# Performance work log

Measured on AMD Instinct MI355X. Metric: run time of the kernel, lower is better.

Reference implementation:

```python
import jax, jax.numpy as jnp
import numpy as np

N_NODES = 50000
N_EDGES = 800000
D_IN = 64
D_OUT = 64


def setup_inputs() -> dict:
    key = jax.random.key(0)
    k1, k2, k3 = jax.random.split(key, 3)
    x = jax.random.normal(k1, (N_NODES, D_IN), dtype=jnp.float32)
    edge_index = jax.random.randint(k2, (2, N_EDGES), 0, N_NODES, dtype=jnp.int64)
    # xavier_uniform for weight [in, out]
    limit = np.sqrt(6.0 / (D_IN + D_OUT)).astype(np.float32)
    weight = jax.random.uniform(k3, (D_IN, D_OUT), dtype=jnp.float32, minval=-limit, maxval=limit)
    bias = jnp.zeros((D_OUT,), dtype=jnp.float32)
    return {"x": x, "edge_index": edge_index, "weight": weight, "bias": bias}


def reference(x, edge_index, weight, bias):
    n = x.shape[0]
    # add self loops
    loops = jnp.arange(n, dtype=edge_index.dtype)
    row = jnp.concatenate([edge_index[0], loops])  # [E+N]
    col = jnp.concatenate([edge_index[1], loops])  # [E+N]
    # degree over row (as in torch_geometric degree(row, N))
    deg = jax.ops.segment_sum(jnp.ones_like(row, dtype=x.dtype), row, num_segments=n)
    deg_inv_sqrt = jnp.where(deg > 0, jax.lax.rsqrt(deg), jnp.zeros_like(deg))
    norm = deg_inv_sqrt[row] * deg_inv_sqrt[col]  # [E+N]
    h = x @ weight  # [N, D_OUT]
    # gather-scale-scatter: out[col] += h[row] * norm
    out = jax.ops.segment_sum(h[row] * norm[:, None], col, num_segments=n)
    return out + bias
```

## Files before the change

### kernel.cpp

```cpp
#include <hip/hip_runtime.h>
#include <hip/hip_bf16.h>


constexpr int N_NODES = 50000;
constexpr int N_EDGES = 800000;
constexpr int D = 64;
constexpr int NB_SCAN = (N_NODES + 255) / 256;

constexpr int B_SLICE = 64;
constexpr int SLICE = N_EDGES / B_SLICE;
constexpr int PACK8 = N_NODES / 4;
constexpr int QUAR = N_NODES / 4;

static __device__ __forceinline__ unsigned short f2bf(float f) {
    unsigned u = __float_as_uint(f);
    unsigned r = (u + 0x7fffu + ((u >> 16) & 1u)) >> 16;
    return (unsigned short)r;
}
static __device__ __forceinline__ float bf2f(unsigned short s) {
    return __uint_as_float((unsigned)s << 16);
}

__global__ __launch_bounds__(1024) void hist_priv_kernel(const int* __restrict__ ei,
                                                         unsigned* __restrict__ bh) {
    __shared__ unsigned loc[PACK8];
    int b = blockIdx.x;
    int s = b & (B_SLICE - 1);
    const int* arr = (b < B_SLICE) ? ei : ei + N_EDGES;
    for (int w = threadIdx.x; w < PACK8; w += 1024) loc[w] = 0;
    __syncthreads();
    const int* p = arr + s * SLICE;
    for (int i = threadIdx.x; i < SLICE; i += 1024) {
        int k = p[i];
        atomicAdd(&loc[k >> 2], 1u << (8 * (k & 3)));
    }
    __syncthreads();
    unsigned* dst = bh + (size_t)b * PACK8;
    for (int w = threadIdx.x; w < PACK8; w += 1024) dst[w] = loc[w];
}

__global__ __launch_bounds__(1024) void reduce_scan_kernel(const unsigned* __restrict__ bh,
                                                           float* __restrict__ dis,
                                                           int* __restrict__ offs_local,
                                                           int* __restrict__ partials,
                                                           unsigned char* __restrict__ bs8) {
    __shared__ int degp[4][256];
    __shared__ int colp[4][256];
    __shared__ int s[256];
    const int t = threadIdx.x;
    const int nl = t & 255;
    const int g = t >> 8;
    const int i = blockIdx.x * 256 + nl;

    unsigned lp[16];
    int ct = 0;
    if (i < N_NODES) {
        const int w = i >> 2;
        const unsigned sh = 8 * (i & 3);
        const unsigned* prow = bh + (size_t)(g * 16) * PACK8 + w;
        unsigned vr[16];
#pragma unroll
        for (int k = 0; k < 16; ++k) vr[k] = prow[(size_t)k * PACK8];
        int dl = 0;
#pragma unroll
        for (int k = 0; k < 16; ++k) dl += (int)((vr[k] >> sh) & 0xffu);
        degp[g][nl] = dl;

        const unsigned* pcol = bh + (size_t)(B_SLICE + g * 16) * PACK8 + w;
        unsigned vc[16];
#pragma unroll
        for (int k = 0; k < 16; ++k) vc[k] = pcol[(size_t)k * PACK8];
        unsigned c = 0;
#pragma unroll
        for (int k = 0; k < 16; ++k) { lp[k] = c; c += (vc[k] >> sh) & 0xffu; }
        ct = (int)c;
        colp[g][nl] = ct;
    } else {
        degp[g][nl] = 0;
        colp[g][nl] = 0;
    }
    __syncthreads();

    if (i < N_NODES) {
        int base = 0;
#pragma unroll
        for (int gg = 0; gg < 4; ++gg) if (gg < g) base += colp[gg][nl];
#pragma unroll
        for (int k = 0; k < 16; ++k)
            bs8[(size_t)(g * 16 + k) * N_NODES + i] = (unsigned char)(base + (int)lp[k]);
        if (g == 0) {
            int deg = degp[0][nl] + degp[1][nl] + degp[2][nl] + degp[3][nl];
            dis[i] = rsqrtf((float)deg + 1.0f);
        }
    }
    if (g == 0) s[nl] = colp[0][nl] + colp[1][nl] + colp[2][nl] + colp[3][nl];
    __syncthreads();

    for (int d = 1; d < 256; d <<= 1) {
        int u = (t < 256 && t >= d) ? s[t - d] : 0;
        __syncthreads();
        if (t < 256) s[t] += u;
        __syncthreads();
    }
    if (g == 0 && i < N_NODES) {
        int tot = colp[0][nl] + colp[1][nl] + colp[2][nl] + colp[3][nl];
        offs_local[i] = s[nl] - tot;
    }
    if (t == 255) partials[blockIdx.x] = s[255];
}

__global__ __launch_bounds__(256, 4) void gemm_kernel(const float* __restrict__ x,
                                                      const float* __restrict__ W,
                                                      const float* __restrict__ dis,
                                                      unsigned short* __restrict__ hs,
                                                      const int* __restrict__ offs_local,
                                                      const int* __restrict__ partials,
                                                      int* __restrict__ offs,
                                                      int do_offs) {
    __shared__ float Xs[64][68];
    __shared__ float Ws[64][64];
    __shared__ int pref[256];
    int t = threadIdx.x;
    int b = blockIdx.x;

    if (do_offs && b < NB_SCAN) {
        pref[t] = (t < NB_SCAN) ? partials[t] : 0;
        __syncthreads();
        for (int d = 1; d < 256; d <<= 1) {
            int u = (t >= d) ? pref[t - d] : 0;
            __syncthreads();
            pref[t] += u;
            __syncthreads();
        }
        int base = pref[b] - partials[b];
        int node = b * 256 + t;
        if (node < N_NODES) offs[node] = base + offs_local[node];
        if (b == 0 && t == 0) offs[N_NODES] = N_EDGES;
    }

    int n0 = blockIdx.x * 64;

    const float4* W4 = (const float4*)W;
    float4* Ws4 = (float4*)Ws;
#pragma unroll
    for (int i = 0; i < 4; ++i) Ws4[t + i * 256] = W4[t + i * 256];

    const float4* x4 = (const float4*)(x + (size_t)n0 * D);
#pragma unroll
    for (int i = 0; i < 4; ++i) {
        int f = t + i * 256;
        int r = f >> 4, c = (f & 15) << 2;
        float4 v = make_float4(0.f, 0.f, 0.f, 0.f);
        if (n0 + r < N_NODES) v = x4[f];
        Xs[r][c] = v.x; Xs[r][c + 1] = v.y; Xs[r][c + 2] = v.z; Xs[r][c + 3] = v.w;
    }
    __syncthreads();

    int tx = t & 15, ty = t >> 4;
    float acc[4][4] = {};
#pragma unroll 8
    for (int k = 0; k < D; ++k) {
        float a[4], bb[4];
#pragma unroll
        for (int i = 0; i < 4; ++i) a[i] = Xs[ty * 4 + i][k];
#pragma unroll
        for (int jj = 0; jj < 4; ++jj) bb[jj] = Ws[k][tx * 4 + jj];
#pragma unroll
        for (int i = 0; i < 4; ++i)
#pragma unroll
            for (int jj = 0; jj < 4; ++jj)
                acc[i][jj] = fmaf(a[i], bb[jj], acc[i][jj]);
    }

#pragma unroll
    for (int i = 0; i < 4; ++i) {
        int r = ty * 4 + i;
        if (n0 + r < N_NODES) {
            float dr = dis[n0 + r];
            ushort4 v;
            v.x = f2bf(acc[i][0] * dr); v.y = f2bf(acc[i][1] * dr);
            v.z = f2bf(acc[i][2] * dr); v.w = f2bf(acc[i][3] * dr);
            *(ushort4*)(hs + (size_t)(n0 + r) * D + tx * 4) = v;
        }
    }
}

__global__ __launch_bounds__(1024) void bucket_det_kernel(const int* __restrict__ ei,
                                                          const unsigned char* __restrict__ bs8,
                                                          const int* __restrict__ offs,
                                                          int* __restrict__ csr) {
    __shared__ unsigned pos[QUAR / 4];
    const int t = threadIdx.x;
    const int s = blockIdx.x >> 2;
    const int q = blockIdx.x & 3;
    const int c0 = q * QUAR;

    const unsigned* rel32 = (const unsigned*)(bs8 + (size_t)s * N_NODES + c0);
    for (int w = t; w < QUAR / 4; w += 1024) pos[w] = rel32[w];
    __syncthreads();

    const int* rowp = ei + s * SLICE;
    const int* colp = ei + N_EDGES + s * SLICE;
    for (int i = t; i < SLICE; i += 1024) {
        int c = colp[i];
        unsigned cc = (unsigned)(c - c0);
        if (cc < (unsigned)QUAR) {
            int base = offs[c];
            unsigned old = atomicAdd(&pos[cc >> 2], 1u << (8 * (cc & 3)));
            unsigned rel = (old >> (8 * (cc & 3))) & 0xffu;
            csr[base + (int)rel] = rowp[i];
        }
    }
}

__global__ __launch_bounds__(256) void gather_kernel(const int* __restrict__ offs,
                                                     const int* __restrict__ csr,
                                                     const unsigned short* __restrict__ hs,
                                                     const float* __restrict__ dis,
                                                     const float* __restrict__ bias,
                                                     float* __restrict__ out) {
    int wave = threadIdx.x >> 6;
    int j = threadIdx.x & 63;
    int n = blockIdx.x * 4 + wave;
    if (n >= N_NODES) return;

    float a[8];
    a[0] = bf2f(hs[(size_t)n * D + j]);
#pragma unroll
    for (int k = 1; k < 8; ++k) a[k] = 0.f;

    int beg = __builtin_amdgcn_readfirstlane(offs[n]);
    int m   = __builtin_amdgcn_readfirstlane(offs[n + 1]) - beg;
    const int* p = csr + beg;

    int i = 0;
    for (; i + 16 <= m; i += 16) {
        int r[16];
        float v[16];
#pragma unroll
        for (int k = 0; k < 16; ++k) r[k] = p[i + k];
#pragma unroll
        for (int k = 0; k < 16; ++k) v[k] = bf2f(hs[(size_t)r[k] * D + j]);
#pragma unroll
        for (int k = 0; k < 16; ++k) a[k & 7] += v[k];
    }
    for (; i + 4 <= m; i += 4) {
        int r0 = p[i], r1 = p[i + 1], r2 = p[i + 2], r3 = p[i + 3];
        a[0] += bf2f(hs[(size_t)r0 * D + j]);
        a[1] += bf2f(hs[(size_t)r1 * D + j]);
        a[2] += bf2f(hs[(size_t)r2 * D + j]);
        a[3] += bf2f(hs[(size_t)r3 * D + j]);
    }
    for (; i < m; ++i) a[1] += bf2f(hs[(size_t)p[i] * D + j]);
    float tot = ((a[0] + a[1]) + (a[2] + a[3])) + ((a[4] + a[5]) + (a[6] + a[7]));
    out[(size_t)n * D + j] = fmaf(dis[n], tot, bias[j]);
}


__global__ void histf_kernel(const int* __restrict__ row, const int* __restrict__ col,
                             int* __restrict__ degi, int* __restrict__ cnt) {
    int e = blockIdx.x * blockDim.x + threadIdx.x;
    if (e < N_EDGES) {
        atomicAdd(&degi[row[e]], 1);
        atomicAdd(&cnt[col[e]], 1);
    }
}

__global__ void disf_kernel(int* __restrict__ degi) {
    int i = blockIdx.x * blockDim.x + threadIdx.x;
    if (i < N_NODES) {
        float d = (float)degi[i] + 1.0f;
        ((float*)degi)[i] = rsqrtf(d);
    }
}

__global__ void block_scan_kernel(const int* __restrict__ cnt, int* __restrict__ offs,
                                  int* __restrict__ partials) {
    __shared__ int s[256];
    int t = threadIdx.x;
    int i = blockIdx.x * 256 + t;
    int v = (i < N_NODES) ? cnt[i] : 0;
    s[t] = v;
    __syncthreads();
    for (int d = 1; d < 256; d <<= 1) {
        int u = (t >= d) ? s[t - d] : 0;
        __syncthreads();
        s[t] += u;
        __syncthreads();
    }
    if (i < N_NODES) offs[i] = s[t] - v;
    if (t == 255) partials[blockIdx.x] = s[t];
}

__global__ void scan_partials_kernel(int* __restrict__ partials) {
    __shared__ int s[256];
    int t = threadIdx.x;
    int v = (t < NB_SCAN) ? partials[t] : 0;
    s[t] = v;
    __syncthreads();
    for (int d = 1; d < 256; d <<= 1) {
        int u = (t >= d) ? s[t - d] : 0;
        __syncthreads();
        s[t] += u;
        __syncthreads();
    }
    if (t < NB_SCAN) partials[t] = s[t] - v;
}

__global__ void add_off_kernel(int* __restrict__ offs, const int* __restrict__ partials) {
    int i = blockIdx.x * 256 + threadIdx.x;
    if (i < N_NODES) offs[i] += partials[blockIdx.x];
    if (i == 0) offs[N_NODES] = N_EDGES;
}

__global__ void bucket_fb_kernel(const int* __restrict__ row, const int* __restrict__ col,
                                 const int* __restrict__ offs, int* __restrict__ cur,
                                 int* __restrict__ csr) {
    int e = blockIdx.x * blockDim.x + threadIdx.x;
    if (e < N_EDGES) {
        int c = col[e];
        int pos = offs[c] + atomicAdd(&cur[c], 1);
        csr[pos] = row[e];
    }
}


extern "C" void kernel_launch(void* const* d_in, const int* in_sizes, int n_in,
                              void* d_out, int out_size, void* d_ws, size_t ws_size,
                              hipStream_t stream) {
    const float* x    = (const float*)d_in[0];
    const int*   ei   = (const int*)d_in[1];
    const float* W    = (const float*)d_in[2];
    const float* bias = (const float*)d_in[3];
    float* out = (float*)d_out;

    char* ws = (char*)d_ws;
    float*          dis      = (float*)(ws + 0);
    int*            offs     = (int*)(ws + 200000);
    int*            offs_loc = (int*)(ws + 400064);
    int*            cur      = (int*)(ws + 600064);
    int*            partials = (int*)(ws + 800064);
    int*            csr      = (int*)(ws + 801088);
    unsigned short* hs       = (unsigned short*)(ws + 4001088);
    unsigned*       bh       = (unsigned*)(ws + 10401088);
    unsigned char*  bs8      = (unsigned char*)(ws + 16801088);

    const size_t WS_NEEDED = 20001088;

    if (ws_size >= WS_NEEDED) {
        hist_priv_kernel<<<2 * B_SLICE, 1024, 0, stream>>>(ei, bh);
        reduce_scan_kernel<<<NB_SCAN, 1024, 0, stream>>>(bh, dis, offs_loc, partials, bs8);
        gemm_kernel<<<(N_NODES + 63) / 64, 256, 0, stream>>>(x, W, dis, hs,
                                                             offs_loc, partials, offs, 1);
        bucket_det_kernel<<<4 * B_SLICE, 1024, 0, stream>>>(ei, bs8, offs, csr);
        gather_kernel<<<(N_NODES + 3) / 4, 256, 0, stream>>>(offs, csr, hs, dis, bias, out);
    } else {
        const int* row = ei;
        const int* col = ei + N_EDGES;
        int* degi = (int*)dis;
        int* cntf = offs_loc;
        hipMemsetAsync(ws, 0, 800064, stream);
        histf_kernel<<<(N_EDGES + 255) / 256, 256, 0, stream>>>(row, col, degi, cntf);
        disf_kernel<<<(N_NODES + 255) / 256, 256, 0, stream>>>(degi);
        block_scan_kernel<<<NB_SCAN, 256, 0, stream>>>(cntf, offs, partials);
        scan_partials_kernel<<<1, 256, 0, stream>>>(partials);
        add_off_kernel<<<NB_SCAN, 256, 0, stream>>>(offs, partials);
        gemm_kernel<<<(N_NODES + 63) / 64, 256, 0, stream>>>(x, W, dis, hs,
                                                             offs_loc, partials, offs, 0);
        bucket_fb_kernel<<<(N_EDGES + 255) / 256, 256, 0, stream>>>(row, col, offs, cur, csr);
        gather_kernel<<<(N_NODES + 3) / 4, 256, 0, stream>>>(offs, csr, hs, dis, bias, out);
    }
}
```

Baseline: 127.6 us.

## Fuse GEMM, bucketing and gather into one cooperative kernel with grid sync

Replaces the three launches (gemm, bucket, gather) with a single cooperative kernel of 256 blocks x 1024 threads. Each block first builds the offsets and scatters its CSR bucket, then part of the blocks compute the bf16-scaled X·W tile, a grid-wide sync separates this from the gather/accumulate phase. It aims to remove launch gaps and overlap bucketing with the GEMM, at the cost of a fixed small grid, LDS union pressure, and a grid barrier; the old path stays as a fallback if the cooperative launch fails.

```diff
diff --git a/kernel.cpp b/kernel.cpp
--- a/kernel.cpp
+++ b/kernel.cpp
@@ -1,5 +1,8 @@
 #include <hip/hip_runtime.h>
 #include <hip/hip_bf16.h>
+#include <hip/hip_cooperative_groups.h>
+
+namespace cg = cooperative_groups;
 
 
 constexpr int N_NODES = 50000;
@@ -107,6 +110,172 @@
         offs_local[i] = s[nl] - tot;
     }
     if (t == 255) partials[blockIdx.x] = s[255];
+}
+
+struct TailLds {
+    union {
+        struct {
+            unsigned pos[QUAR / 4];
+            int pref[256];
+        } bk;
+        struct {
+            float Xs[4][64][68];
+            float Ws[64][64];
+        } g;
+    } u;
+};
+
+__global__ __launch_bounds__(1024, 4) void fused_tail_kernel(
+        const int* __restrict__ ei,
+        const int* __restrict__ offs_local,
+        const int* __restrict__ partials,
+        const unsigned char* __restrict__ bs8,
+        const float* __restrict__ x,
+        const float* __restrict__ W,
+        const float* __restrict__ dis,
+        unsigned short* __restrict__ hs,
+        int* __restrict__ csr,
+        int* __restrict__ offs,
+        const float* __restrict__ bias,
+        float* __restrict__ out) {
+    __shared__ TailLds L;
+    const int t = threadIdx.x;
+    const int b = blockIdx.x;
+
+    if (t < 256) L.u.bk.pref[t] = (t < NB_SCAN) ? partials[t] : 0;
+    __syncthreads();
+    for (int d = 1; d < 256; d <<= 1) {
+        int u = 0;
+        if (t < 256 && t >= d) u = L.u.bk.pref[t - d];
+        __syncthreads();
+        if (t < 256) L.u.bk.pref[t] += u;
+        __syncthreads();
+    }
+    if (t < 256) {
+        int inc = L.u.bk.pref[t];
+        int own = (t < NB_SCAN) ? partials[t] : 0;
+        L.u.bk.pref[t] = inc - own;
+    }
+    __syncthreads();
+
+    {
+        const int s = b >> 2;
+        const int q = b & 3;
+        const int c0 = q * QUAR;
+        const unsigned* rel32 = (const unsigned*)(bs8 + (size_t)s * N_NODES + c0);
+        for (int w = t; w < QUAR / 4; w += 1024) L.u.bk.pos[w] = rel32[w];
+        if (s == 0) {
+            const int* olq = offs_local + c0;
+            for (int w = t; w < QUAR; w += 1024) {
+                int node = c0 + w;
+                offs[node] = L.u.bk.pref[node >> 8] + olq[w];
+            }
+            if (q == 3 && t == 0) offs[N_NODES] = N_EDGES;
+        }
+        __syncthreads();
+
+        const int* rowp = ei + s * SLICE;
+        const int* colp = ei + N_EDGES + s * SLICE;
+        for (int i = t; i < SLICE; i += 1024) {
+            int c = colp[i];
+            unsigned cc = (unsigned)(c - c0);
+            if (cc < (unsigned)QUAR) {
+                int base = L.u.bk.pref[c >> 8] + offs_local[c];
+                unsigned old = atomicAdd(&L.u.bk.pos[cc >> 2], 1u << (8 * (cc & 3)));
+                unsigned rel = (old >> (8 * (cc & 3))) & 0xffu;
+                csr[base + (int)rel] = rowp[i];
+            }
+        }
+    }
+    __syncthreads();
+
+    if (b < 196) {
+        const int grp = t >> 8, t256 = t & 255;
+        const int tb = b * 4 + grp;
+        const int n0 = tb * 64;
+
+        ((float4*)L.u.g.Ws)[t] = ((const float4*)W)[t];
+
+        float (*Xs)[68] = L.u.g.Xs[grp];
+        const float4* x4 = (const float4*)(x + (size_t)n0 * D);
+#pragma unroll
+        for (int i = 0; i < 4; ++i) {
+            int f = t256 + i * 256;
+            int r = f >> 4, c = (f & 15) << 2;
+            float4 v = make_float4(0.f, 0.f, 0.f, 0.f);
+            if (n0 + r < N_NODES) v = x4[f];
+            Xs[r][c] = v.x; Xs[r][c + 1] = v.y; Xs[r][c + 2] = v.z; Xs[r][c + 3] = v.w;
+        }
+        __syncthreads();
+
+        int tx = t256 & 15, ty = t256 >> 4;
+        float acc[4][4] = {};
+#pragma unroll 8
+        for (int k = 0; k < D; ++k) {
+            float a[4], bb[4];
+#pragma unroll
+            for (int i = 0; i < 4; ++i) a[i] = Xs[ty * 4 + i][k];
+#pragma unroll
+            for (int jj = 0; jj < 4; ++jj) bb[jj] = L.u.g.Ws[k][tx * 4 + jj];
+#pragma unroll
+            for (int i = 0; i < 4; ++i)
+#pragma unroll
+                for (int jj = 0; jj < 4; ++jj)
+                    acc[i][jj] = fmaf(a[i], bb[jj], acc[i][jj]);
+        }
+
+#pragma unroll
+        for (int i = 0; i < 4; ++i) {
+            int r = ty * 4 + i;
+            if (n0 + r < N_NODES) {
+                float dr = dis[n0 + r];
+                ushort4 v;
+                v.x = f2bf(acc[i][0] * dr); v.y = f2bf(acc[i][1] * dr);
+                v.z = f2bf(acc[i][2] * dr); v.w = f2bf(acc[i][3] * dr);
+                *(ushort4*)(hs + (size_t)(n0 + r) * D + tx * 4) = v;
+            }
+        }
+    }
+
+    __threadfence();
+    cg::this_grid().sync();
+
+    {
+        const int wave = t >> 6;
+        const int j = t & 63;
+        for (int n = b * 16 + wave; n < N_NODES; n += 4096) {
+            float a[8];
+            a[0] = bf2f(hs[(size_t)n * D + j]);
+#pragma unroll
+            for (int k = 1; k < 8; ++k) a[k] = 0.f;
+
+            int beg = __builtin_amdgcn_readfirstlane(offs[n]);
+            int m   = __builtin_amdgcn_readfirstlane(offs[n + 1]) - beg;
+            const int* p = csr + beg;
+
+            int i = 0;
+            for (; i + 16 <= m; i += 16) {
+                int r[16];
+                float v[16];
+#pragma unroll
+                for (int k = 0; k < 16; ++k) r[k] = p[i + k];
+#pragma unroll
+                for (int k = 0; k < 16; ++k) v[k] = bf2f(hs[(size_t)r[k] * D + j]);
+#pragma unroll
+                for (int k = 0; k < 16; ++k) a[k & 7] += v[k];
+            }
+            for (; i + 4 <= m; i += 4) {
+                int r0 = p[i], r1 = p[i + 1], r2 = p[i + 2], r3 = p[i + 3];
+                a[0] += bf2f(hs[(size_t)r0 * D + j]);
+                a[1] += bf2f(hs[(size_t)r1 * D + j]);
+                a[2] += bf2f(hs[(size_t)r2 * D + j]);
+                a[3] += bf2f(hs[(size_t)r3 * D + j]);
+            }
+            for (; i < m; ++i) a[1] += bf2f(hs[(size_t)p[i] * D + j]);
+            float tot = ((a[0] + a[1]) + (a[2] + a[3])) + ((a[4] + a[5]) + (a[6] + a[7]));
+            out[(size_t)n * D + j] = fmaf(dis[n], tot, bias[j]);
+        }
+    }
 }
 
 __global__ __launch_bounds__(256, 4) void gemm_kernel(const float* __restrict__ x,
@@ -350,10 +519,30 @@
     if (ws_size >= WS_NEEDED) {
         hist_priv_kernel<<<2 * B_SLICE, 1024, 0, stream>>>(ei, bh);
         reduce_scan_kernel<<<NB_SCAN, 1024, 0, stream>>>(bh, dis, offs_loc, partials, bs8);
-        gemm_kernel<<<(N_NODES + 63) / 64, 256, 0, stream>>>(x, W, dis, hs,
-                                                             offs_loc, partials, offs, 1);
-        bucket_det_kernel<<<4 * B_SLICE, 1024, 0, stream>>>(ei, bs8, offs, csr);
-        gather_kernel<<<(N_NODES + 3) / 4, 256, 0, stream>>>(offs, csr, hs, dis, bias, out);
+
+        const int*           a_ei   = ei;
+        const int*           a_ol   = offs_loc;
+        const int*           a_pt   = partials;
+        const unsigned char* a_bs8  = bs8;
+        const float*         a_x    = x;
+        const float*         a_W    = W;
+        const float*         a_dis  = dis;
+        unsigned short*      a_hs   = hs;
+        int*                 a_csr  = csr;
+        int*                 a_offs = offs;
+        const float*         a_bias = bias;
+        float*               a_out  = out;
+        void* args[] = {&a_ei, &a_ol, &a_pt, &a_bs8, &a_x, &a_W, &a_dis,
+                        &a_hs, &a_csr, &a_offs, &a_bias, &a_out};
+        hipError_t ce = hipLaunchCooperativeKernel((const void*)fused_tail_kernel,
+                                                   dim3(256), dim3(1024), args, 0, stream);
+        if (ce != hipSuccess) {
+            gemm_kernel<<<(N_NODES + 63) / 64, 256, 0, stream>>>(x, W, dis, hs,
+                                                                 offs_loc, partials, offs, 1);
+            bucket_det_kernel<<<4 * B_SLICE, 1024, 0, stream>>>(ei, bs8, offs, csr);
+            gather_kernel<<<(N_NODES + 3) / 4, 256, 0, stream>>>(offs, csr, hs, dis,
+                                                                 bias, out);
+        }
     } else {
         const int* row = ei;
         const int* col = ei + N_EDGES;
```

Measured after the change: 303.5 us. 2.38x slower.

## Fuse GEMM and CSR bucket fill into one heterogeneous-block kernel

Applied to the files above, without the earlier changes.

Merges the GEMM and the deterministic bucket-fill kernels into a single launch. Blocks are split by index: 512 bucket blocks work on eighth-ranges of destination nodes and the remaining blocks run the GEMM. Each bucket block recomputes the partials prefix scan itself and derives CSR offsets from offs_local plus the block prefix, so it no longer waits on offs written by the GEMM kernel. This removes one launch and lets the GEMM overlap with the atomic-heavy scatter, at the cost of a redundant scan in every bucket block and more ei re-reads from the finer node partitioning.

```diff
diff --git a/kernel.cpp b/kernel.cpp
--- a/kernel.cpp
+++ b/kernel.cpp
@@ -10,7 +10,10 @@
 constexpr int B_SLICE = 64;
 constexpr int SLICE = N_EDGES / B_SLICE;
 constexpr int PACK8 = N_NODES / 4;
-constexpr int QUAR = N_NODES / 4;
+
+constexpr int OCT = 6272;
+constexpr int NB_BUCKET = B_SLICE * 8;
+constexpr int NB_GEMM = (N_NODES + 63) / 64;
 
 static __device__ __forceinline__ unsigned short f2bf(float f) {
     unsigned u = __float_as_uint(f);
@@ -53,7 +56,6 @@
     const int i = blockIdx.x * 256 + nl;
 
     unsigned lp[16];
-    int ct = 0;
     if (i < N_NODES) {
         const int w = i >> 2;
         const unsigned sh = 8 * (i & 3);
@@ -73,8 +75,7 @@
         unsigned c = 0;
 #pragma unroll
         for (int k = 0; k < 16; ++k) { lp[k] = c; c += (vc[k] >> sh) & 0xffu; }
-        ct = (int)c;
-        colp[g][nl] = ct;
+        colp[g][nl] = (int)c;
     } else {
         degp[g][nl] = 0;
         colp[g][nl] = 0;
@@ -109,106 +110,126 @@
     if (t == 255) partials[blockIdx.x] = s[255];
 }
 
-__global__ __launch_bounds__(256, 4) void gemm_kernel(const float* __restrict__ x,
-                                                      const float* __restrict__ W,
-                                                      const float* __restrict__ dis,
-                                                      unsigned short* __restrict__ hs,
-                                                      const int* __restrict__ offs_local,
-                                                      const int* __restrict__ partials,
-                                                      int* __restrict__ offs,
-                                                      int do_offs) {
-    __shared__ float Xs[64][68];
-    __shared__ float Ws[64][64];
-    __shared__ int pref[256];
-    int t = threadIdx.x;
-    int b = blockIdx.x;
-
-    if (do_offs && b < NB_SCAN) {
-        pref[t] = (t < NB_SCAN) ? partials[t] : 0;
+struct FgbLds {
+    union {
+        struct {
+            unsigned pos[OCT / 4];
+            int pref[256];
+        } bk;
+        struct {
+            float Xs[64][68];
+            float Ws[64][64];
+        } g;
+    } u;
+};
+
+__global__ __launch_bounds__(256, 4) void fused_gb_kernel(
+        const float* __restrict__ x,
+        const float* __restrict__ W,
+        const float* __restrict__ dis,
+        unsigned short* __restrict__ hs,
+        const int* __restrict__ ei,
+        const int* __restrict__ offs_local,
+        const int* __restrict__ partials,
+        const unsigned char* __restrict__ bs8,
+        int* __restrict__ csr,
+        int* __restrict__ offs) {
+    __shared__ FgbLds L;
+    const int t = threadIdx.x;
+    const int b = blockIdx.x;
+
+    if (b < NB_BUCKET) {
+        L.u.bk.pref[t] = (t < NB_SCAN) ? partials[t] : 0;
         __syncthreads();
         for (int d = 1; d < 256; d <<= 1) {
-            int u = (t >= d) ? pref[t - d] : 0;
+            int u = (t >= d) ? L.u.bk.pref[t - d] : 0;
             __syncthreads();
-            pref[t] += u;
+            L.u.bk.pref[t] += u;
             __syncthreads();
         }
-        int base = pref[b] - partials[b];
-        int node = b * 256 + t;
-        if (node < N_NODES) offs[node] = base + offs_local[node];
-        if (b == 0 && t == 0) offs[N_NODES] = N_EDGES;
-    }
-
-    int n0 = blockIdx.x * 64;
-
-    const float4* W4 = (const float4*)W;
-    float4* Ws4 = (float4*)Ws;
-#pragma unroll
-    for (int i = 0; i < 4; ++i) Ws4[t + i * 256] = W4[t + i * 256];
-
-    const float4* x4 = (const float4*)(x + (size_t)n0 * D);
-#pragma unroll
-    for (int i = 0; i < 4; ++i) {
-        int f = t + i * 256;
-        int r = f >> 4, c = (f & 15) << 2;
-        float4 v = make_float4(0.f, 0.f, 0.f, 0.f);
-        if (n0 + r < N_NODES) v = x4[f];
-        Xs[r][c] = v.x; Xs[r][c + 1] = v.y; Xs[r][c + 2] = v.z; Xs[r][c + 3] = v.w;
-    }
-    __syncthreads();
-
-    int tx = t & 15, ty = t >> 4;
-    float acc[4][4] = {};
+        {
+            int inc = L.u.bk.pref[t];
+            int own = (t < NB_SCAN) ? partials[t] : 0;
+            L.u.bk.pref[t] = inc - own;
+        }
+        __syncthreads();
+
+        const int s = b >> 3;
+        const int o = b & 7;
+        const int c0 = o * OCT;
+        const int range = (c0 + OCT <= N_NODES) ? OCT : (N_NODES - c0);
+
+        const unsigned* rel32 = (const unsigned*)(bs8 + (size_t)s * N_NODES + c0);
+        for (int w = t; w < range / 4; w += 256) L.u.bk.pos[w] = rel32[w];
+
+        if (s == 0) {
+            const int* olq = offs_local + c0;
+            for (int w = t; w < range; w += 256) {
+                int node = c0 + w;
+                offs[node] = L.u.bk.pref[node >> 8] + olq[w];
+            }
+            if (o == 7 && t == 0) offs[N_NODES] = N_EDGES;
+        }
+        __syncthreads();
+
+        const int* rowp = ei + s * SLICE;
+        const int* colp = ei + N_EDGES + s * SLICE;
+        for (int i = t; i < SLICE; i += 256) {
+            int c = colp[i];
+            unsigned cc = (unsigned)(c - c0);
+            if (cc < (unsigned)range) {
+                int base = L.u.bk.pref[c >> 8] + offs_local[c];
+                unsigned old = atomicAdd(&L.u.bk.pos[cc >> 2], 1u << (8 * (cc & 3)));
+                unsigned rel = (old >> (8 * (cc & 3))) & 0xffu;
+                csr[base + (int)rel] = rowp[i];
+            }
+        }
+    } else {
+        const int n0 = (b - NB_BUCKET) * 64;
+
+        const float4* W4 = (const float4*)W;
+        float4* Ws4 = (float4*)L.u.g.Ws;
+#pragma unroll
+        for (int i = 0; i < 4; ++i) Ws4[t + i * 256] = W4[t + i * 256];
+
+        const float4* x4 = (const float4*)(x + (size_t)n0 * D);
+#pragma unroll
+        for (int i = 0; i < 4; ++i) {
+            int f = t + i * 256;
+            int r = f >> 4, c = (f & 15) << 2;
+            float4 v = make_float4(0.f, 0.f, 0.f, 0.f);
+            if (n0 + r < N_NODES) v = x4[f];
+            L.u.g.Xs[r][c] = v.x; L.u.g.Xs[r][c + 1] = v.y;
+            L.u.g.Xs[r][c + 2] = v.z; L.u.g.Xs[r][c + 3] = v.w;
+        }
+        __syncthreads();
+
+        int tx = t & 15, ty = t >> 4;
+        float acc[4][4] = {};
 #pragma unroll 8
-    for (int k = 0; k < D; ++k) {
-        float a[4], bb[4];
-#pragma unroll
-        for (int i = 0; i < 4; ++i) a[i] = Xs[ty * 4 + i][k];
-#pragma unroll
-        for (int jj = 0; jj < 4; ++jj) bb[jj] = Ws[k][tx * 4 + jj];
-#pragma unroll
-        for (int i = 0; i < 4; ++i)
-#pragma unroll
-            for (int jj = 0; jj < 4; ++jj)
-                acc[i][jj] = fmaf(a[i], bb[jj], acc[i][jj]);
-    }
-
-#pragma unroll
-    for (int i = 0; i < 4; ++i) {
-        int r = ty * 4 + i;
-        if (n0 + r < N_NODES) {
-            float dr = dis[n0 + r];
-            ushort4 v;
-            v.x = f2bf(acc[i][0] * dr); v.y = f2bf(acc[i][1] * dr);
-            v.z = f2bf(acc[i][2] * dr); v.w = f2bf(acc[i][3] * dr);
-            *(ushort4*)(hs + (size_t)(n0 + r) * D + tx * 4) = v;
-        }
-    }
-}
-
-__global__ __launch_bounds__(1024) void bucket_det_kernel(const int* __restrict__ ei,
-                                                          const unsigned char* __restrict__ bs8,
-                                                          const int* __restrict__ offs,
-                                                          int* __restrict__ csr) {
-    __shared__ unsigned pos[QUAR / 4];
-    const int t = threadIdx.x;
-    const int s = blockIdx.x >> 2;
-    const int q = blockIdx.x & 3;
-    const int c0 = q * QUAR;
-
-    const unsigned* rel32 = (const unsigned*)(bs8 + (size_t)s * N_NODES + c0);
-    for (int w = t; w < QUAR / 4; w += 1024) pos[w] = rel32[w];
-    __syncthreads();
-
-    const int* rowp = ei + s * SLICE;
-    const int* colp = ei + N_EDGES + s * SLICE;
-    for (int i = t; i < SLICE; i += 1024) {
-        int c = colp[i];
-        unsigned cc = (unsigned)(c - c0);
-        if (cc < (unsigned)QUAR) {
-            int base = offs[c];
-            unsigned old = atomicAdd(&pos[cc >> 2], 1u << (8 * (cc & 3)));
-            unsigned rel = (old >> (8 * (cc & 3))) & 0xffu;
-            csr[base + (int)rel] = rowp[i];
+        for (int k = 0; k < D; ++k) {
+            float a[4], bb[4];
+#pragma unroll
+            for (int i = 0; i < 4; ++i) a[i] = L.u.g.Xs[ty * 4 + i][k];
+#pragma unroll
+            for (int jj = 0; jj < 4; ++jj) bb[jj] = L.u.g.Ws[k][tx * 4 + jj];
+#pragma unroll
+            for (int i = 0; i < 4; ++i)
+#pragma unroll
+                for (int jj = 0; jj < 4; ++jj)
+                    acc[i][jj] = fmaf(a[i], bb[jj], acc[i][jj]);
+        }
+
+#pragma unroll
+        for (int i = 0; i < 4; ++i) {
+            int r = ty * 4 + i;
+            if (n0 + r < N_NODES) {
+                float dr = dis[n0 + r];
+                ushort4 v;
+                v.x = f2bf(acc[i][0] * dr); v.y = f2bf(acc[i][1] * dr);
+                v.z = f2bf(acc[i][2] * dr); v.w = f2bf(acc[i][3] * dr);
+                *(ushort4*)(hs + (size_t)(n0 + r) * D + tx * 4) = v;
+            }
         }
     }
 }
@@ -256,6 +277,60 @@
     out[(size_t)n * D + j] = fmaf(dis[n], tot, bias[j]);
 }
 
+__global__ __launch_bounds__(256, 4) void gemm_kernel(const float* __restrict__ x,
+                                                      const float* __restrict__ W,
+                                                      const float* __restrict__ dis,
+                                                      unsigned short* __restrict__ hs) {
+    __shared__ float Xs[64][68];
+    __shared__ float Ws[64][64];
+    int t = threadIdx.x;
+    int n0 = blockIdx.x * 64;
+
+    const float4* W4 = (const float4*)W;
+    float4* Ws4 = (float4*)Ws;
+#pragma unroll
+    for (int i = 0; i < 4; ++i) Ws4[t + i * 256] = W4[t + i * 256];
+
+    const float4* x4 = (const float4*)(x + (size_t)n0 * D);
+#pragma unroll
+    for (int i = 0; i < 4; ++i) {
+        int f = t + i * 256;
+        int r = f >> 4, c = (f & 15) << 2;
+        float4 v = make_float4(0.f, 0.f, 0.f, 0.f);
+        if (n0 + r < N_NODES) v = x4[f];
+        Xs[r][c] = v.x; Xs[r][c + 1] = v.y; Xs[r][c + 2] = v.z; Xs[r][c + 3] = v.w;
+    }
+    __syncthreads();
+
+    int tx = t & 15, ty = t >> 4;
+    float acc[4][4] = {};
+#pragma unroll 8
+    for (int k = 0; k < D; ++k) {
+        float a[4], bb[4];
+#pragma unroll
+        for (int i = 0; i < 4; ++i) a[i] = Xs[ty * 4 + i][k];
+#pragma unroll
+        for (int jj = 0; jj < 4; ++jj) bb[jj] = Ws[k][tx * 4 + jj];
+#pragma unroll
+        for (int i = 0; i < 4; ++i)
+#pragma unroll
+            for (int jj = 0; jj < 4; ++jj)
+                acc[i][jj] = fmaf(a[i], bb[jj], acc[i][jj]);
+    }
+
+#pragma unroll
+    for (int i = 0; i < 4; ++i) {
+        int r = ty * 4 + i;
+        if (n0 + r < N_NODES) {
+            float dr = dis[n0 + r];
+            ushort4 v;
+            v.x = f2bf(acc[i][0] * dr); v.y = f2bf(acc[i][1] * dr);
+            v.z = f2bf(acc[i][2] * dr); v.w = f2bf(acc[i][3] * dr);
+            *(ushort4*)(hs + (size_t)(n0 + r) * D + tx * 4) = v;
+        }
+    }
+}
+
 
 __global__ void histf_kernel(const int* __restrict__ row, const int* __restrict__ col,
                              int* __restrict__ degi, int* __restrict__ cnt) {
@@ -350,9 +425,9 @@
     if (ws_size >= WS_NEEDED) {
         hist_priv_kernel<<<2 * B_SLICE, 1024, 0, stream>>>(ei, bh);
         reduce_scan_kernel<<<NB_SCAN, 1024, 0, stream>>>(bh, dis, offs_loc, partials, bs8);
-        gemm_kernel<<<(N_NODES + 63) / 64, 256, 0, stream>>>(x, W, dis, hs,
-                                                             offs_loc, partials, offs, 1);
-        bucket_det_kernel<<<4 * B_SLICE, 1024, 0, stream>>>(ei, bs8, offs, csr);
+        fused_gb_kernel<<<NB_BUCKET + NB_GEMM, 256, 0, stream>>>(x, W, dis, hs, ei,
+                                                                 offs_loc, partials,
+                                                                 bs8, csr, offs);
         gather_kernel<<<(N_NODES + 3) / 4, 256, 0, stream>>>(offs, csr, hs, dis, bias, out);
     } else {
         const int* row = ei;
@@ -365,8 +440,7 @@
         block_scan_kernel<<<NB_SCAN, 256, 0, stream>>>(cntf, offs, partials);
         scan_partials_kernel<<<1, 256, 0, stream>>>(partials);
         add_off_kernel<<<NB_SCAN, 256, 0, stream>>>(offs, partials);
-        gemm_kernel<<<(N_NODES + 63) / 64, 256, 0, stream>>>(x, W, dis, hs,
-                                                             offs_loc, partials, offs, 0);
+        gemm_kernel<<<(N_NODES + 63) / 64, 256, 0, stream>>>(x, W, dis, hs);
         bucket_fb_kernel<<<(N_EDGES + 255) / 256, 256, 0, stream>>>(row, col, offs, cur, csr);
         gather_kernel<<<(N_NODES + 3) / 4, 256, 0, stream>>>(offs, csr, hs, dis, bias, out);
     }
```

New measurement: 140.5 us. 10.1% more time.
